# Kernel tuning notes

Measured on AMD Instinct MI355X. Metric: run time of the kernel, lower is better.

## Reference

```python
import jax, jax.numpy as jnp
import numpy as np

PAD = 1
NMS_DIST = 4
BORDER_DIST = 4
TOP_K = 500
DET_THRESH = 0.8


def _conv(x, w, b, pad):
    y = jax.lax.conv_general_dilated(
        x, w, window_strides=(1, 1), padding=[(pad, pad), (pad, pad)],
        dimension_numbers=("NCHW", "OIHW", "NCHW"))
    return y + b[None, :, None, None]


def setup_inputs() -> dict:
    key = jax.random.key(0)
    ks = jax.random.split(key, 10)
    B, C, H, W = 2, 1, 384, 384

    def w(k, o, i, s):
        return jax.random.normal(k, (o, i, s, s), jnp.float32) * (1.0 / np.sqrt(i * s * s))

    return {
        "images": jax.random.uniform(ks[0], (B, C, H, W), jnp.float32),
        "bb_w1": w(ks[1], 64, 1, 3), "bb_b1": jnp.zeros((64,), jnp.float32),
        "bb_w2": w(ks[2], 64, 64, 3), "bb_b2": jnp.zeros((64,), jnp.float32),
        "bb_w3": w(ks[3], 128, 64, 3), "bb_b3": jnp.zeros((128,), jnp.float32),
        "bb_w4": w(ks[4], 128, 128, 3), "bb_b4": jnp.zeros((128,), jnp.float32),
        "det_w1": w(ks[5], 128, 128, 3), "det_b1": jnp.zeros((128,), jnp.float32),
        "det_w2": w(ks[6], 1, 128, 1), "det_b2": jnp.zeros((1,), jnp.float32),
        "des_w1": w(ks[7], 256, 128, 3), "des_b1": jnp.zeros((256,), jnp.float32),
        "des_w2": w(ks[8], 128, 256, 1), "des_b2": jnp.zeros((128,), jnp.float32),
        "scale_factor": jnp.float32(1.0),
    }


def reference(images, bb_w1, bb_b1, bb_w2, bb_b2, bb_w3, bb_b3, bb_w4, bb_b4,
              det_w1, det_b1, det_w2, det_b2, des_w1, des_b1, des_w2, des_b2,
              scale_factor):
    relu = jax.nn.relu
    x = relu(_conv(images, bb_w1, bb_b1, PAD))
    x = relu(_conv(x, bb_w2, bb_b2, PAD))
    x = relu(_conv(x, bb_w3, bb_b3, PAD))
    feats = relu(_conv(x, bb_w4, bb_b4, PAD))  # [B,128,H,W]

    # Detector head: 3x3 conv+ReLU, then 1x1 conv -> logits [B,1,H,W]
    d = relu(_conv(feats, det_w1, det_b1, PAD))
    logits = _conv(d, det_w2, det_b2, 0)

    # Descriptor head: 3x3 conv+ReLU (lat=256), then 1x1 conv -> raw descriptors [B,D,H,W]
    e = relu(_conv(feats, des_w1, des_b1, PAD))
    raw = _conv(e, des_w2, des_b2, 0)

    # MagicPoint post-processing (cell_size=1): prob = sigmoid(logits)
    prob = jax.nn.sigmoid(logits[:, 0])  # [B,H,W]
    B, H, W = prob.shape

    # Box NMS via max-pool: keep local maxima above threshold, suppress borders
    win = 2 * NMS_DIST + 1
    pooled = jax.lax.reduce_window(prob, -jnp.inf, jax.lax.max,
                                   (1, win, win), (1, 1, 1), "SAME")
    ys = jnp.arange(H)
    xs = jnp.arange(W)
    border = ((ys >= BORDER_DIST) & (ys < H - BORDER_DIST))[:, None] \
           & ((xs >= BORDER_DIST) & (xs < W - BORDER_DIST))[None, :]
    nms_prob = jnp.where((prob >= pooled) & (prob > DET_THRESH) & border, prob, 0.0)

    # Fixed top-k keypoints per image
    flat = nms_prob.reshape(B, H * W)
    topv, topi = jax.lax.top_k(flat, TOP_K)  # [B,K]
    y = (topi // W).astype(jnp.float32)
    xp = (topi % W).astype(jnp.float32)
    positions = jnp.stack([y, xp, topv], axis=-1)  # [B,K,3] (row, col, prob)

    # sparsify_descriptors: gather raw descriptors at keypoint locations, L2-normalize
    D = raw.shape[1]
    raw_flat = raw.reshape(B, D, H * W)
    desc = jnp.take_along_axis(raw_flat, topi[:, None, :], axis=2)  # [B,D,K]
    desc = jnp.swapaxes(desc, 1, 2)  # [B,K,D]
    norm = jnp.maximum(jnp.linalg.norm(desc, axis=-1, keepdims=True), 1e-12)
    sparse_descriptors = scale_factor * desc / norm
    return sparse_descriptors, positions
```

## Files before the change

kernel.cpp:

```cpp
#include <hip/hip_runtime.h>
#include <hip/hip_bf16.h>

#define DEVI __device__ __forceinline__

typedef __bf16 bf16x8 __attribute__((ext_vector_type(8)));
typedef float  f32x4  __attribute__((ext_vector_type(4)));
typedef unsigned short ushort_t;

static constexpr int H = 384, W = 384, BATCH = 2, HW = H * W;
static constexpr int NMSD = 4, BORD = 4, TOPK = 500;
static constexpr float THRESH = 0.8f;
static constexpr int CAP = 2048;
static constexpr int SORTN = 2048;

DEVI ushort_t f2b(float f) {
  __hip_bfloat16 h = __float2bfloat16(f);
  ushort_t s;
  __builtin_memcpy(&s, &h, 2);
  return s;
}
DEVI float b2f(ushort_t u) { return __uint_as_float(((unsigned)u) << 16); }

DEVI void gload_lds16(const void* g, void* l) {
  __builtin_amdgcn_global_load_lds((const __attribute__((address_space(1))) void*)g,
                                   (__attribute__((address_space(3))) void*)l,
                                   16, 0, 0);
}

__global__ void init_ws(ushort_t* zer, int* cnt) {
  int t = threadIdx.x;
  if (t < 512) zer[t] = 0;
  if (t < 2) cnt[t] = 0;
}

__global__ void repack_w(const float* __restrict__ src, ushort_t* __restrict__ dst,
                         int O, int I) {
  int n = O * I * 9;
  for (int d = blockIdx.x * blockDim.x + threadIdx.x; d < n; d += gridDim.x * blockDim.x) {
    int t = d / (O * I);
    int r = d % (O * I);
    int o = r / I, i = r % I;
    dst[d] = f2b(src[(o * I + i) * 9 + t]);
  }
}

__global__ void repack_dw1(const float* __restrict__ src, ushort_t* __restrict__ dst) {
  int d = blockIdx.x * 256 + threadIdx.x;
  if (d >= 256 * 1152) return;
  int o = d / 1152, k = d % 1152;
  dst[(size_t)(k >> 2) * 1024 + o * 4 + (k & 3)] = f2b(src[d]);
}

__global__ void repack_dw2(const float* __restrict__ src, float* __restrict__ dst) {
  int d = blockIdx.x * 256 + threadIdx.x;
  if (d >= 256 * 128) return;
  int o = d / 128, c = d % 128;
  dst[d] = src[c * 256 + o];
}

__global__ __launch_bounds__(256) void conv1_kernel(
    const float* __restrict__ img, const float* __restrict__ w,
    const float* __restrict__ bias, ushort_t* __restrict__ xout) {
  __shared__ __align__(16) float wt[9 * 64];
  __shared__ float bs[64];
  const int tid = threadIdx.x;
  for (int j = tid; j < 576; j += 256) {
    int co = j / 9, t = j % 9;
    wt[t * 64 + co] = w[j];
  }
  if (tid < 64) bs[tid] = bias[tid];
  __syncthreads();

  const int p = blockIdx.x * 256 + tid;
  const int b = p / HW, rem = p % HW;
  const int y = rem / W, x = rem % W;

  float in[9];
#pragma unroll
  for (int t = 0; t < 9; ++t) {
    int yy = y + t / 3 - 1, xx = x + t % 3 - 1;
    in[t] = (yy >= 0 && yy < H && xx >= 0 && xx < W) ? img[(size_t)b * HW + yy * W + xx] : 0.f;
  }
  float acc[64];
#pragma unroll
  for (int c = 0; c < 64; ++c) acc[c] = bs[c];
#pragma unroll
  for (int t = 0; t < 9; ++t) {
    float v = in[t];
#pragma unroll
    for (int c4 = 0; c4 < 16; ++c4) {
      float4 w4 = *reinterpret_cast<const float4*>(&wt[t * 64 + c4 * 4]);
      acc[c4 * 4 + 0] += w4.x * v;
      acc[c4 * 4 + 1] += w4.y * v;
      acc[c4 * 4 + 2] += w4.z * v;
      acc[c4 * 4 + 3] += w4.w * v;
    }
  }
  ushort_t* op = xout + (size_t)p * 64;
#pragma unroll
  for (int g = 0; g < 8; ++g) {
    uint4 u;
    u.x = (unsigned)f2b(fmaxf(acc[g * 8 + 0], 0.f)) | ((unsigned)f2b(fmaxf(acc[g * 8 + 1], 0.f)) << 16);
    u.y = (unsigned)f2b(fmaxf(acc[g * 8 + 2], 0.f)) | ((unsigned)f2b(fmaxf(acc[g * 8 + 3], 0.f)) << 16);
    u.z = (unsigned)f2b(fmaxf(acc[g * 8 + 4], 0.f)) | ((unsigned)f2b(fmaxf(acc[g * 8 + 5], 0.f)) << 16);
    u.w = (unsigned)f2b(fmaxf(acc[g * 8 + 6], 0.f)) | ((unsigned)f2b(fmaxf(acc[g * 8 + 7], 0.f)) << 16);
    *reinterpret_cast<uint4*>(op + g * 8) = u;
  }
}

template <int CIN, int COUT, int MFRAG, int NFRAG>
__global__ __launch_bounds__(256) void conv3x3_mfma(
    const ushort_t* __restrict__ xin, const ushort_t* __restrict__ wp,
    const float* __restrict__ bias, ushort_t* __restrict__ xout,
    const ushort_t* __restrict__ zer) {
  constexpr int NT = 128;
  constexpr int BROWS = 144;
  constexpr int ACH3 = 3 * COUT / 16;
  constexpr int APW = ACH3 / 4;

  __shared__ __align__(16) ushort_t lA[3 * COUT * 32];
  __shared__ __align__(16) ushort_t lB[BROWS * 32];

  const int x0 = (blockIdx.x % (W / NT)) * NT;
  const int y = blockIdx.x / (W / NT);
  const int b = blockIdx.y;

  const int tid = threadIdx.x;
  const int wid = tid >> 6, lane = tid & 63;
  const int wr = wid >> 1, wc = wid & 1;
  const int l4 = lane >> 2;
  const int lb8 = (lane & 3) * 8;
  const int kg = lane >> 4;
  const int lr = lane & 15;

  const f32x4 fz = {0.f, 0.f, 0.f, 0.f};
  f32x4 acc[MFRAG][NFRAG];
#pragma unroll
  for (int m = 0; m < MFRAG; ++m)
#pragma unroll
    for (int n = 0; n < NFRAG; ++n) acc[m][n] = fz;

#pragma unroll 1
  for (int dy = -1; dy <= 1; ++dy) {
    const int yy = y + dy;
    const bool rowok = (yy >= 0) && (yy < H);
    const ushort_t* srow = xin + ((size_t)(b * H + yy) * W) * CIN;
#pragma unroll 1
    for (int cc = 0; cc < CIN; cc += 32) {
#pragma unroll
      for (int j = 0; j < APW; ++j) {
        int ch = wid * APW + j;
        int row = ch * 16 + l4;
        int tt = row / COUT, co = row % COUT;
        const ushort_t* src =
            wp + ((size_t)((dy + 1) * 3 + tt) * COUT + co) * CIN + cc + lb8;
        gload_lds16(src, &lA[ch * 512]);
      }
      for (int ch = wid; ch < 9; ch += 4) {
        int row = ch * 16 + l4;
        int xx = x0 - 1 + row;
        const ushort_t* src = (rowok && row < 130 && xx >= 0 && xx < W)
                                  ? srow + (size_t)xx * CIN + cc + lb8
                                  : zer + lb8;
        gload_lds16(src, &lB[ch * 512]);
      }
      __syncthreads();
#pragma unroll
      for (int tt = 0; tt < 3; ++tt) {
        bf16x8 af[MFRAG], bfr[NFRAG];
#pragma unroll
        for (int m = 0; m < MFRAG; ++m)
          af[m] = *reinterpret_cast<const bf16x8*>(
              &lA[(tt * COUT + wr * MFRAG * 16 + m * 16 + lr) * 32 + kg * 8]);
#pragma unroll
        for (int n = 0; n < NFRAG; ++n)
          bfr[n] = *reinterpret_cast<const bf16x8*>(
              &lB[(wc * NFRAG * 16 + n * 16 + lr + tt) * 32 + kg * 8]);
#pragma unroll
        for (int m = 0; m < MFRAG; ++m)
#pragma unroll
          for (int n = 0; n < NFRAG; ++n)
            acc[m][n] = __builtin_amdgcn_mfma_f32_16x16x32_bf16(af[m], bfr[n], acc[m][n], 0, 0, 0);
      }
      __syncthreads();
    }
  }

  const int lq = lane >> 4;
  ushort_t* orow = xout + ((size_t)(b * H + y) * W) * COUT;
#pragma unroll
  for (int m = 0; m < MFRAG; ++m) {
    const int co = wr * MFRAG * 16 + m * 16 + lq * 4;
    const float4 bv = *reinterpret_cast<const float4*>(&bias[co]);
#pragma unroll
    for (int n = 0; n < NFRAG; ++n) {
      const int px = x0 + wc * NFRAG * 16 + n * 16 + lr;
      f32x4 v = acc[m][n];
      ushort4 pk;
      pk.x = f2b(fmaxf(v[0] + bv.x, 0.f));
      pk.y = f2b(fmaxf(v[1] + bv.y, 0.f));
      pk.z = f2b(fmaxf(v[2] + bv.z, 0.f));
      pk.w = f2b(fmaxf(v[3] + bv.w, 0.f));
      *reinterpret_cast<ushort4*>(&orow[(size_t)px * COUT + co]) = pk;
    }
  }
}

__global__ __launch_bounds__(256) void det2_sigmoid(
    const ushort_t* __restrict__ dbuf, const float* __restrict__ w2,
    const float* __restrict__ b2, float* __restrict__ prob) {
  __shared__ float ws[128];
  const int tid = threadIdx.x;
  if (tid < 128) ws[tid] = w2[tid];
  __syncthreads();
  const int p = blockIdx.x * 256 + tid;
  const ushort_t* dp = dbuf + (size_t)p * 128;
  float acc = b2[0];
#pragma unroll
  for (int k = 0; k < 128; k += 8) {
    uint4 q = *reinterpret_cast<const uint4*>(dp + k);
    acc += __uint_as_float(q.x << 16) * ws[k + 0];
    acc += __uint_as_float(q.x & 0xffff0000u) * ws[k + 1];
    acc += __uint_as_float(q.y << 16) * ws[k + 2];
    acc += __uint_as_float(q.y & 0xffff0000u) * ws[k + 3];
    acc += __uint_as_float(q.z << 16) * ws[k + 4];
    acc += __uint_as_float(q.z & 0xffff0000u) * ws[k + 5];
    acc += __uint_as_float(q.w << 16) * ws[k + 6];
    acc += __uint_as_float(q.w & 0xffff0000u) * ws[k + 7];
  }
  prob[p] = 1.f / (1.f + expf(-acc));
}

__global__ __launch_bounds__(256) void rowmax9(const float* __restrict__ prob,
                                               float* __restrict__ tmp) {
  const int p = blockIdx.x * 256 + threadIdx.x;
  const int x = p % W;
  float m = -1e30f;
#pragma unroll
  for (int d = -NMSD; d <= NMSD; ++d) {
    int xx = x + d;
    if (xx >= 0 && xx < W) m = fmaxf(m, prob[p + d]);
  }
  tmp[p] = m;
}

__global__ __launch_bounds__(256) void colmax9_cand(
    const float* __restrict__ tmp, const float* __restrict__ prob,
    int* __restrict__ cnt, float* __restrict__ candv, int* __restrict__ candi) {
  const int p = blockIdx.x * 256 + threadIdx.x;
  const int b = p / HW, rem = p % HW;
  const int y = rem / W, x = rem % W;
  float m = -1e30f;
#pragma unroll
  for (int d = -NMSD; d <= NMSD; ++d) {
    int yy = y + d;
    if (yy >= 0 && yy < H) m = fmaxf(m, tmp[(size_t)b * HW + yy * W + x]);
  }
  float pv = prob[p];
  bool keep = (pv >= m) && (pv > THRESH) &&
              (y >= BORD) && (y < H - BORD) && (x >= BORD) && (x < W - BORD);
  if (keep) {
    int pos = atomicAdd(&cnt[b], 1);
    if (pos < CAP) {
      candv[b * CAP + pos] = pv;
      candi[b * CAP + pos] = rem;
    }
  }
}

__global__ __launch_bounds__(256) void select_topk(
    const int* __restrict__ cnt, const float* __restrict__ candv,
    const int* __restrict__ candi, float* __restrict__ pos_out,
    int* __restrict__ topi_g) {
  __shared__ float sv[SORTN];
  __shared__ int si[SORTN];
  __shared__ int tail[TOPK];
  const int b = blockIdx.x, tid = threadIdx.x;
  int nc = cnt[b];
  if (nc > CAP) nc = CAP;
  for (int j = tid; j < SORTN; j += 256) {
    if (j < nc) {
      sv[j] = candv[b * CAP + j];
      si[j] = candi[b * CAP + j];
    } else {
      sv[j] = -1.f;
      si[j] = 0x7fffffff;
    }
  }
  __syncthreads();
  if (nc > 0) {
    for (int k = 2; k <= SORTN; k <<= 1) {
      for (int j = k >> 1; j > 0; j >>= 1) {
        for (int i = tid; i < SORTN; i += 256) {
          int l = i ^ j;
          if (l > i) {
            float vi = sv[i], vl = sv[l];
            int ii = si[i], il = si[l];
            bool i_better = (vi > vl) || (vi == vl && ii < il);
            bool desc = ((i & k) == 0);
            bool sw = desc ? (!i_better) : i_better;
            if (sw) {
              sv[i] = vl; sv[l] = vi;
              si[i] = il; si[l] = ii;
            }
          }
        }
        __syncthreads();
      }
    }
  }
  if (tid == 0) {
    int need = TOPK - nc;
    if (need < 0) need = 0;
    int idx = 0, filled = 0;
    while (filled < need && idx < HW) {
      bool used = false;
      for (int q = 0; q < nc; ++q)
        if (si[q] == idx) { used = true; break; }
      if (!used) tail[filled++] = idx;
      ++idx;
    }
  }
  __syncthreads();
  for (int k2 = tid; k2 < TOPK; k2 += 256) {
    float v; int idx;
    if (k2 < nc) { v = sv[k2]; idx = si[k2]; }
    else         { v = 0.f;    idx = tail[k2 - nc]; }
    pos_out[((size_t)b * TOPK + k2) * 3 + 0] = (float)(idx / W);
    pos_out[((size_t)b * TOPK + k2) * 3 + 1] = (float)(idx % W);
    pos_out[((size_t)b * TOPK + k2) * 3 + 2] = v;
    topi_g[b * TOPK + k2] = idx;
  }
}

__global__ __launch_bounds__(256) void des_head(
    const ushort_t* __restrict__ feats, const int* __restrict__ topi_g,
    const ushort_t* __restrict__ w1t, const float* __restrict__ b1,
    const float* __restrict__ w2t, const float* __restrict__ b2,
    const float* __restrict__ scale, float* __restrict__ desc_out) {
  __shared__ __align__(16) float xf[1152];
  __shared__ __align__(16) float es[256];
  __shared__ float rs[128];
  __shared__ float nrm_s;
  const int g = blockIdx.x;
  const int b = g / TOPK;
  const int tid = threadIdx.x;
  const int idx = topi_g[g];
  const int y = idx / W, x = idx % W;
  for (int j = tid; j < 1152; j += 256) {
    int ci = j / 9, t = j % 9;
    int yy = y + t / 3 - 1, xx = x + t % 3 - 1;
    xf[j] = (yy >= 0 && yy < H && xx >= 0 && xx < W)
                ? b2f(feats[((size_t)(b * H + yy) * W + xx) * 128 + ci])
                : 0.f;
  }
  __syncthreads();
  float e = b1[tid];
  const ushort4* w4p = reinterpret_cast<const ushort4*>(w1t);
#pragma unroll 4
  for (int k4 = 0; k4 < 288; ++k4) {
    ushort4 wv = w4p[(size_t)k4 * 256 + tid];
    float4 x4 = *reinterpret_cast<const float4*>(&xf[k4 * 4]);
    e += b2f(wv.x) * x4.x + b2f(wv.y) * x4.y + b2f(wv.z) * x4.z + b2f(wv.w) * x4.w;
  }
  es[tid] = fmaxf(e, 0.f);
  __syncthreads();
  if (tid < 128) {
    float r = b2[tid];
#pragma unroll 4
    for (int o = 0; o < 256; ++o) r += es[o] * w2t[o * 128 + tid];
    rs[tid] = r;
  }
  __syncthreads();
  if (tid < 64) {
    float v = rs[tid] * rs[tid] + rs[tid + 64] * rs[tid + 64];
    for (int off = 32; off > 0; off >>= 1) v += __shfl_down(v, off);
    if (tid == 0) nrm_s = sqrtf(v);
  }
  __syncthreads();
  if (tid < 128) {
    float nrm = fmaxf(nrm_s, 1e-12f);
    desc_out[(size_t)g * 128 + tid] = rs[tid] * (scale[0] / nrm);
  }
}

extern "C" void kernel_launch(void* const* d_in, const int* in_sizes, int n_in,
                              void* d_out, int out_size, void* d_ws, size_t ws_size,
                              hipStream_t stream) {
  (void)in_sizes; (void)n_in; (void)out_size; (void)ws_size;
  const float* images = (const float*)d_in[0];
  const float* bbw1 = (const float*)d_in[1];  const float* bbb1 = (const float*)d_in[2];
  const float* bbw2 = (const float*)d_in[3];  const float* bbb2 = (const float*)d_in[4];
  const float* bbw3 = (const float*)d_in[5];  const float* bbb3 = (const float*)d_in[6];
  const float* bbw4 = (const float*)d_in[7];  const float* bbb4 = (const float*)d_in[8];
  const float* dtw1 = (const float*)d_in[9];  const float* dtb1 = (const float*)d_in[10];
  const float* dtw2 = (const float*)d_in[11]; const float* dtb2 = (const float*)d_in[12];
  const float* dsw1 = (const float*)d_in[13]; const float* dsb1 = (const float*)d_in[14];
  const float* dsw2 = (const float*)d_in[15]; const float* dsb2 = (const float*)d_in[16];
  const float* scale = (const float*)d_in[17];

  char* ws = (char*)d_ws;
  constexpr size_t SZ64 = (size_t)BATCH * HW * 64 * 2;
  constexpr size_t SZ128 = (size_t)BATCH * HW * 128 * 2;

  ushort_t* x1   = (ushort_t*)ws;
  ushort_t* x2   = (ushort_t*)(ws + SZ64);
  ushort_t* x3   = (ushort_t*)(ws + SZ128);
  ushort_t* fts  = (ushort_t*)ws;
  ushort_t* dbuf = (ushort_t*)(ws + SZ128);

  size_t off = 2 * SZ128;
  auto alloc = [&](size_t bytes) {
    char* p = ws + off;
    off = (off + bytes + 255) & ~(size_t)255;
    return p;
  };
  float* prob = (float*)alloc((size_t)BATCH * HW * 4);
  float* tmp  = (float*)alloc((size_t)BATCH * HW * 4);
  ushort_t* wp2 = (ushort_t*)alloc(9 * 64 * 64 * 2);
  ushort_t* wp3 = (ushort_t*)alloc(9 * 128 * 64 * 2);
  ushort_t* wp4 = (ushort_t*)alloc(9 * 128 * 128 * 2);
  ushort_t* wpd = (ushort_t*)alloc(9 * 128 * 128 * 2);
  ushort_t* w1t = (ushort_t*)alloc(288 * 256 * 4 * 2);
  float*    w2t = (float*)alloc(256 * 128 * 4);
  ushort_t* zer = (ushort_t*)alloc(1024);
  int* cnt      = (int*)alloc(256);
  float* candv  = (float*)alloc((size_t)BATCH * CAP * 4);
  int* candi    = (int*)alloc((size_t)BATCH * CAP * 4);
  int* topi_g   = (int*)alloc((size_t)BATCH * TOPK * 4);

  float* desc_out = (float*)d_out;
  float* pos_out  = (float*)d_out + (size_t)BATCH * TOPK * 128;

  init_ws<<<1, 512, 0, stream>>>(zer, cnt);
  repack_w<<<64, 256, 0, stream>>>(bbw2, wp2, 64, 64);
  repack_w<<<64, 256, 0, stream>>>(bbw3, wp3, 128, 64);
  repack_w<<<128, 256, 0, stream>>>(bbw4, wp4, 128, 128);
  repack_w<<<128, 256, 0, stream>>>(dtw1, wpd, 128, 128);
  repack_dw1<<<1152, 256, 0, stream>>>(dsw1, w1t);
  repack_dw2<<<128, 256, 0, stream>>>(dsw2, w2t);

  conv1_kernel<<<BATCH * HW / 256, 256, 0, stream>>>(images, bbw1, bbb1, x1);
  conv3x3_mfma<64, 64, 2, 4><<<dim3(3 * H, BATCH), 256, 0, stream>>>(x1, wp2, bbb2, x2, zer);
  conv3x3_mfma<64, 128, 4, 4><<<dim3(3 * H, BATCH), 256, 0, stream>>>(x2, wp3, bbb3, x3, zer);
  conv3x3_mfma<128, 128, 4, 4><<<dim3(3 * H, BATCH), 256, 0, stream>>>(x3, wp4, bbb4, fts, zer);
  conv3x3_mfma<128, 128, 4, 4><<<dim3(3 * H, BATCH), 256, 0, stream>>>(fts, wpd, dtb1, dbuf, zer);

  det2_sigmoid<<<BATCH * HW / 256, 256, 0, stream>>>(dbuf, dtw2, dtb2, prob);
  rowmax9<<<BATCH * HW / 256, 256, 0, stream>>>(prob, tmp);
  colmax9_cand<<<BATCH * HW / 256, 256, 0, stream>>>(tmp, prob, cnt, candv, candi);
  select_topk<<<BATCH, 256, 0, stream>>>(cnt, candv, candi, pos_out, topi_g);
  des_head<<<BATCH * TOPK, 256, 0, stream>>>(fts, topi_g, w1t, dsb1, w2t, dsb2, scale, desc_out);
}
```

Measured before the change: 537.0 us.

## Restructure conv MFMA kernel with register weights and double-buffered LDS

Weights are repacked into an MFMA-fragment layout so each wave loads A fragments directly from global memory into registers instead of staging them through LDS. The conv kernel now tiles 192 pixels per block, with each wave covering all output channels and 48 pixels. The input tile is double-buffered in LDS across a flattened (dy, channel-chunk) loop, which needs one barrier per step instead of two. The weight-repack kernels are merged into one launch, and the detector 1x1, sigmoid and row max are fused into one kernel using LDS. The trade-off is more registers per wave for the accumulators and repeated global or L2 traffic for weights.

```diff
diff --git a/kernel.cpp b/kernel.cpp
--- a/kernel.cpp
+++ b/kernel.cpp
@@ -27,35 +27,45 @@
                                    16, 0, 0);
 }
 
-__global__ void init_ws(ushort_t* zer, int* cnt) {
-  int t = threadIdx.x;
-  if (t < 512) zer[t] = 0;
-  if (t < 2) cnt[t] = 0;
-}
-
-__global__ void repack_w(const float* __restrict__ src, ushort_t* __restrict__ dst,
-                         int O, int I) {
-  int n = O * I * 9;
-  for (int d = blockIdx.x * blockDim.x + threadIdx.x; d < n; d += gridDim.x * blockDim.x) {
-    int t = d / (O * I);
-    int r = d % (O * I);
-    int o = r / I, i = r % I;
-    dst[d] = f2b(src[(o * I + i) * 9 + t]);
-  }
-}
-
-__global__ void repack_dw1(const float* __restrict__ src, ushort_t* __restrict__ dst) {
+DEVI void wfrag_one(const float* __restrict__ src, ushort_t* __restrict__ dst,
+                    int d, int COC, int CCC, int CIN) {
+  int j = d & 7, l = (d >> 3) & 63, rest = d >> 9;
+  int ccc = rest % CCC;
+  int t2 = rest / CCC;
+  int coc = t2 % COC, t = t2 / COC;
+  int co = coc * 16 + (l & 15), ci = ccc * 32 + (l >> 4) * 8 + j;
+  dst[d] = f2b(src[((size_t)co * CIN + ci) * 9 + t]);
+}
+
+__global__ __launch_bounds__(256) void setup_all(
+    const float* __restrict__ w2s, ushort_t* __restrict__ wp2,
+    const float* __restrict__ w3s, ushort_t* __restrict__ wp3,
+    const float* __restrict__ w4s, ushort_t* __restrict__ wp4,
+    const float* __restrict__ wds, ushort_t* __restrict__ wpd,
+    const float* __restrict__ dw1, ushort_t* __restrict__ w1t,
+    const float* __restrict__ dw2, float* __restrict__ w2t,
+    ushort_t* __restrict__ zer, int* __restrict__ cnt) {
   int d = blockIdx.x * 256 + threadIdx.x;
-  if (d >= 256 * 1152) return;
-  int o = d / 1152, k = d % 1152;
-  dst[(size_t)(k >> 2) * 1024 + o * 4 + (k & 3)] = f2b(src[d]);
-}
-
-__global__ void repack_dw2(const float* __restrict__ src, float* __restrict__ dst) {
-  int d = blockIdx.x * 256 + threadIdx.x;
-  if (d >= 256 * 128) return;
-  int o = d / 128, c = d % 128;
-  dst[d] = src[c * 256 + o];
+  if (d < 1024) { zer[d] = 0; if (d < 2) cnt[d] = 0; return; }
+  d -= 1024;
+  if (d < 36864)  { wfrag_one(w2s, wp2, d, 4, 2, 64);  return; }
+  d -= 36864;
+  if (d < 73728)  { wfrag_one(w3s, wp3, d, 8, 2, 64);  return; }
+  d -= 73728;
+  if (d < 147456) { wfrag_one(w4s, wp4, d, 8, 4, 128); return; }
+  d -= 147456;
+  if (d < 147456) { wfrag_one(wds, wpd, d, 8, 4, 128); return; }
+  d -= 147456;
+  if (d < 294912) {
+    int o = d / 1152, k = d % 1152;
+    w1t[(size_t)(k >> 2) * 1024 + o * 4 + (k & 3)] = f2b(dw1[d]);
+    return;
+  }
+  d -= 294912;
+  if (d < 32768) {
+    int o = d / 128, c = d % 128;
+    w2t[d] = dw2[c * 256 + o];
+  }
 }
 
 __global__ __launch_bounds__(256) void conv1_kernel(
@@ -108,18 +118,20 @@
   }
 }
 
-template <int CIN, int COUT, int MFRAG, int NFRAG>
+template <int CIN, int COUT>
 __global__ __launch_bounds__(256) void conv3x3_mfma(
     const ushort_t* __restrict__ xin, const ushort_t* __restrict__ wp,
     const float* __restrict__ bias, ushort_t* __restrict__ xout,
     const ushort_t* __restrict__ zer) {
-  constexpr int NT = 128;
-  constexpr int BROWS = 144;
-  constexpr int ACH3 = 3 * COUT / 16;
-  constexpr int APW = ACH3 / 4;
-
-  __shared__ __align__(16) ushort_t lA[3 * COUT * 32];
-  __shared__ __align__(16) ushort_t lB[BROWS * 32];
+  constexpr int NT = 192;
+  constexpr int MFRAG = COUT / 16;
+  constexpr int NFRAG = 3;
+  constexpr int CC = CIN / 32;
+  constexpr int COC = COUT / 16;
+  constexpr int P = 3 * CC;
+  constexpr int BCH = 13;
+
+  __shared__ __align__(16) ushort_t lB[2][BCH * 512];
 
   const int x0 = (blockIdx.x % (W / NT)) * NT;
   const int y = blockIdx.x / (W / NT);
@@ -127,7 +139,7 @@
 
   const int tid = threadIdx.x;
   const int wid = tid >> 6, lane = tid & 63;
-  const int wr = wid >> 1, wc = wid & 1;
+  const int wc = wid;
   const int l4 = lane >> 2;
   const int lb8 = (lane & 3) * 8;
   const int kg = lane >> 4;
@@ -140,49 +152,46 @@
 #pragma unroll
     for (int n = 0; n < NFRAG; ++n) acc[m][n] = fz;
 
+  auto stage = [&](int p) {
+    const int dyi = p / CC, ccc = p % CC, pb = p & 1;
+    const int yy = y + dyi - 1;
+    const bool rowok = (yy >= 0) && (yy < H);
+    const ushort_t* srow = xin + ((size_t)(b * H + yy) * W) * CIN + ccc * 32;
+    for (int ch = wid; ch < BCH; ch += 4) {
+      int row = ch * 16 + l4;
+      int xx = x0 - 1 + row;
+      const ushort_t* src = (rowok && row < 194 && xx >= 0 && xx < W)
+                                ? srow + (size_t)xx * CIN + lb8
+                                : zer + lb8;
+      gload_lds16(src, &lB[pb][ch * 512]);
+    }
+  };
+
+  stage(0);
 #pragma unroll 1
-  for (int dy = -1; dy <= 1; ++dy) {
-    const int yy = y + dy;
-    const bool rowok = (yy >= 0) && (yy < H);
-    const ushort_t* srow = xin + ((size_t)(b * H + yy) * W) * CIN;
-#pragma unroll 1
-    for (int cc = 0; cc < CIN; cc += 32) {
-#pragma unroll
-      for (int j = 0; j < APW; ++j) {
-        int ch = wid * APW + j;
-        int row = ch * 16 + l4;
-        int tt = row / COUT, co = row % COUT;
-        const ushort_t* src =
-            wp + ((size_t)((dy + 1) * 3 + tt) * COUT + co) * CIN + cc + lb8;
-        gload_lds16(src, &lA[ch * 512]);
-      }
-      for (int ch = wid; ch < 9; ch += 4) {
-        int row = ch * 16 + l4;
-        int xx = x0 - 1 + row;
-        const ushort_t* src = (rowok && row < 130 && xx >= 0 && xx < W)
-                                  ? srow + (size_t)xx * CIN + cc + lb8
-                                  : zer + lb8;
-        gload_lds16(src, &lB[ch * 512]);
-      }
-      __syncthreads();
-#pragma unroll
-      for (int tt = 0; tt < 3; ++tt) {
-        bf16x8 af[MFRAG], bfr[NFRAG];
-#pragma unroll
-        for (int m = 0; m < MFRAG; ++m)
-          af[m] = *reinterpret_cast<const bf16x8*>(
-              &lA[(tt * COUT + wr * MFRAG * 16 + m * 16 + lr) * 32 + kg * 8]);
+  for (int p = 0; p < P; ++p) {
+    __syncthreads();
+    if (p + 1 < P) stage(p + 1);
+    const int dyi = p / CC, ccc = p % CC, pb = p & 1;
+    const ushort_t* wbase = wp + ((size_t)(dyi * 3) * COC * CC + ccc) * 512 + lane * 8;
+    const ushort_t* lbb = &lB[pb][0];
+#pragma unroll
+    for (int tt = 0; tt < 3; ++tt) {
+      bf16x8 af[MFRAG];
+#pragma unroll
+      for (int m = 0; m < MFRAG; ++m)
+        af[m] = *reinterpret_cast<const bf16x8*>(
+            wbase + ((size_t)tt * COC * CC + m * CC) * 512);
+      bf16x8 bfr[NFRAG];
+#pragma unroll
+      for (int n = 0; n < NFRAG; ++n)
+        bfr[n] = *reinterpret_cast<const bf16x8*>(
+            &lbb[(wc * 48 + n * 16 + lr + tt) * 32 + kg * 8]);
+#pragma unroll
+      for (int m = 0; m < MFRAG; ++m)
 #pragma unroll
         for (int n = 0; n < NFRAG; ++n)
-          bfr[n] = *reinterpret_cast<const bf16x8*>(
-              &lB[(wc * NFRAG * 16 + n * 16 + lr + tt) * 32 + kg * 8]);
-#pragma unroll
-        for (int m = 0; m < MFRAG; ++m)
-#pragma unroll
-          for (int n = 0; n < NFRAG; ++n)
-            acc[m][n] = __builtin_amdgcn_mfma_f32_16x16x32_bf16(af[m], bfr[n], acc[m][n], 0, 0, 0);
-      }
-      __syncthreads();
+          acc[m][n] = __builtin_amdgcn_mfma_f32_16x16x32_bf16(af[m], bfr[n], acc[m][n], 0, 0, 0);
     }
   }
 
@@ -190,11 +199,11 @@
   ushort_t* orow = xout + ((size_t)(b * H + y) * W) * COUT;
 #pragma unroll
   for (int m = 0; m < MFRAG; ++m) {
-    const int co = wr * MFRAG * 16 + m * 16 + lq * 4;
+    const int co = m * 16 + lq * 4;
     const float4 bv = *reinterpret_cast<const float4*>(&bias[co]);
 #pragma unroll
     for (int n = 0; n < NFRAG; ++n) {
-      const int px = x0 + wc * NFRAG * 16 + n * 16 + lr;
+      const int px = x0 + wc * 48 + n * 16 + lr;
       f32x4 v = acc[m][n];
       ushort4 pk;
       pk.x = f2b(fmaxf(v[0] + bv.x, 0.f));
@@ -206,14 +215,16 @@
   }
 }
 
-__global__ __launch_bounds__(256) void det2_sigmoid(
+__global__ __launch_bounds__(384) void det2_rowmax(
     const ushort_t* __restrict__ dbuf, const float* __restrict__ w2,
-    const float* __restrict__ b2, float* __restrict__ prob) {
+    const float* __restrict__ b2, float* __restrict__ prob,
+    float* __restrict__ tmp) {
   __shared__ float ws[128];
+  __shared__ float pr[W];
   const int tid = threadIdx.x;
   if (tid < 128) ws[tid] = w2[tid];
   __syncthreads();
-  const int p = blockIdx.x * 256 + tid;
+  const int p = blockIdx.x * W + tid;
   const ushort_t* dp = dbuf + (size_t)p * 128;
   float acc = b2[0];
 #pragma unroll
@@ -228,18 +239,15 @@
     acc += __uint_as_float(q.w << 16) * ws[k + 6];
     acc += __uint_as_float(q.w & 0xffff0000u) * ws[k + 7];
   }
-  prob[p] = 1.f / (1.f + expf(-acc));
-}
-
-__global__ __launch_bounds__(256) void rowmax9(const float* __restrict__ prob,
-                                               float* __restrict__ tmp) {
-  const int p = blockIdx.x * 256 + threadIdx.x;
-  const int x = p % W;
+  float pv = 1.f / (1.f + expf(-acc));
+  prob[p] = pv;
+  pr[tid] = pv;
+  __syncthreads();
   float m = -1e30f;
 #pragma unroll
   for (int d = -NMSD; d <= NMSD; ++d) {
-    int xx = x + d;
-    if (xx >= 0 && xx < W) m = fmaxf(m, prob[p + d]);
+    int xx = tid + d;
+    if (xx >= 0 && xx < W) m = fmaxf(m, pr[xx]);
   }
   tmp[p] = m;
 }
@@ -423,7 +431,7 @@
   ushort_t* wpd = (ushort_t*)alloc(9 * 128 * 128 * 2);
   ushort_t* w1t = (ushort_t*)alloc(288 * 256 * 4 * 2);
   float*    w2t = (float*)alloc(256 * 128 * 4);
-  ushort_t* zer = (ushort_t*)alloc(1024);
+  ushort_t* zer = (ushort_t*)alloc(2048);
   int* cnt      = (int*)alloc(256);
   float* candv  = (float*)alloc((size_t)BATCH * CAP * 4);
   int* candi    = (int*)alloc((size_t)BATCH * CAP * 4);
@@ -432,22 +440,16 @@
   float* desc_out = (float*)d_out;
   float* pos_out  = (float*)d_out + (size_t)BATCH * TOPK * 128;
 
-  init_ws<<<1, 512, 0, stream>>>(zer, cnt);
-  repack_w<<<64, 256, 0, stream>>>(bbw2, wp2, 64, 64);
-  repack_w<<<64, 256, 0, stream>>>(bbw3, wp3, 128, 64);
-  repack_w<<<128, 256, 0, stream>>>(bbw4, wp4, 128, 128);
-  repack_w<<<128, 256, 0, stream>>>(dtw1, wpd, 128, 128);
-  repack_dw1<<<1152, 256, 0, stream>>>(dsw1, w1t);
-  repack_dw2<<<128, 256, 0, stream>>>(dsw2, w2t);
+  setup_all<<<2868, 256, 0, stream>>>(bbw2, wp2, bbw3, wp3, bbw4, wp4, dtw1, wpd,
+                                      dsw1, w1t, dsw2, w2t, zer, cnt);
 
   conv1_kernel<<<BATCH * HW / 256, 256, 0, stream>>>(images, bbw1, bbb1, x1);
-  conv3x3_mfma<64, 64, 2, 4><<<dim3(3 * H, BATCH), 256, 0, stream>>>(x1, wp2, bbb2, x2, zer);
-  conv3x3_mfma<64, 128, 4, 4><<<dim3(3 * H, BATCH), 256, 0, stream>>>(x2, wp3, bbb3, x3, zer);
-  conv3x3_mfma<128, 128, 4, 4><<<dim3(3 * H, BATCH), 256, 0, stream>>>(x3, wp4, bbb4, fts, zer);
-  conv3x3_mfma<128, 128, 4, 4><<<dim3(3 * H, BATCH), 256, 0, stream>>>(fts, wpd, dtb1, dbuf, zer);
-
-  det2_sigmoid<<<BATCH * HW / 256, 256, 0, stream>>>(dbuf, dtw2, dtb2, prob);
-  rowmax9<<<BATCH * HW / 256, 256, 0, stream>>>(prob, tmp);
+  conv3x3_mfma<64, 64>  <<<dim3(2 * H, BATCH), 256, 0, stream>>>(x1, wp2, bbb2, x2, zer);
+  conv3x3_mfma<64, 128> <<<dim3(2 * H, BATCH), 256, 0, stream>>>(x2, wp3, bbb3, x3, zer);
+  conv3x3_mfma<128, 128><<<dim3(2 * H, BATCH), 256, 0, stream>>>(x3, wp4, bbb4, fts, zer);
+  conv3x3_mfma<128, 128><<<dim3(2 * H, BATCH), 256, 0, stream>>>(fts, wpd, dtb1, dbuf, zer);
+
+  det2_rowmax<<<BATCH * H, 384, 0, stream>>>(dbuf, dtw2, dtb2, prob, tmp);
   colmax9_cand<<<BATCH * HW / 256, 256, 0, stream>>>(tmp, prob, cnt, candv, candi);
   select_topk<<<BATCH, 256, 0, stream>>>(cnt, candv, candi, pos_out, topi_g);
   des_head<<<BATCH * TOPK, 256, 0, stream>>>(fts, topi_g, w1t, dsb1, w2t, dsb2, scale, desc_out);
```

Measured after the change: 567.6 us. 5.7% more time.
